# Kernel optimization log

Measured on AMD Instinct MI355X. Metric: run time of the kernel, lower is better.

Reference implementation:

```python
import jax, jax.numpy as jnp
import numpy as np

B, L, D_MODEL, H, D_K, D_V, C = 4, 2048, 512, 8, 64, 64, 5
LN_EPS = 1e-5


def setup_inputs() -> dict:
    key = jax.random.key(0)
    ks = jax.random.split(key, 9)
    u_k = min(int(C * np.log(L)), L)  # 38
    s = 1.0 / np.sqrt(D_MODEL)
    return {
        "input_Q": jax.random.normal(ks[0], (B, L, D_MODEL), jnp.float32),
        "input_K": jax.random.normal(ks[1], (B, L, D_MODEL), jnp.float32),
        "input_V": jax.random.normal(ks[2], (B, L, D_MODEL), jnp.float32),
        "W_Q": jax.random.normal(ks[3], (D_MODEL, H * D_K), jnp.float32) * s,
        "W_K": jax.random.normal(ks[4], (D_MODEL, H * D_K), jnp.float32) * s,
        "W_V": jax.random.normal(ks[5], (D_MODEL, H * D_V), jnp.float32) * s,
        "W_fc": jax.random.normal(ks[6], (H * D_V, D_MODEL), jnp.float32) * (1.0 / np.sqrt(H * D_V)),
        "ln_gamma": jnp.ones((D_MODEL,), jnp.float32),
        "ln_beta": jnp.zeros((D_MODEL,), jnp.float32),
        "index_sample": jax.random.randint(ks[7], (L, u_k), 0, L, jnp.int32),
    }


def reference(input_Q, input_K, input_V, W_Q, W_K, W_V, W_fc, ln_gamma, ln_beta, index_sample):
    Bb, L_Q, _ = input_Q.shape
    L_K = input_K.shape[1]
    u_q = min(int(C * np.log(L_Q)), L_Q)  # n_top queries kept

    # projections -> (B, H, L, d)
    Q = (input_Q @ W_Q).reshape(Bb, L_Q, H, D_K).transpose(0, 2, 1, 3)
    K = (input_K @ W_K).reshape(Bb, L_K, H, D_K).transpose(0, 2, 1, 3)
    V = (input_V @ W_V).reshape(Bb, L_K, H, D_V).transpose(0, 2, 1, 3)

    # sampled QK scores: gather u_k random keys per query position
    K_sample = K[:, :, index_sample, :]                      # (B,H,L_Q,u_k,d_k)
    QK_sample = jnp.einsum('bhqe,bhqke->bhqk', Q, K_sample)  # (B,H,L_Q,u_k)

    # sparsity measure M = max - mean, top-u_q queries
    M = QK_sample.max(axis=-1) - QK_sample.mean(axis=-1)     # (B,H,L_Q)
    _, idx = jax.lax.top_k(M, u_q)                           # (B,H,u_q)

    # attention only for selected queries
    Q_sel = jnp.take_along_axis(Q, idx[..., None], axis=2)   # (B,H,u_q,d_k)
    scores = jnp.einsum('bhue,bhke->bhuk', Q_sel, K) / np.sqrt(D_K)
    attn = jax.nn.softmax(scores, axis=-1)
    values = jnp.einsum('bhuk,bhkd->bhud', attn, V)          # (B,H,u_q,d_v)

    # initial context = mean of V (attn_mask is None), scatter selected rows
    context = jnp.broadcast_to(V.mean(axis=2, keepdims=True), (Bb, H, L_Q, D_V))
    bb = jnp.arange(Bb)[:, None, None]
    hh = jnp.arange(H)[None, :, None]
    context = context.at[bb, hh, idx].set(values)

    context = context.transpose(0, 2, 1, 3).reshape(Bb, L_Q, H * D_V)
    out = context @ W_fc                                     # dropout p=0.0

    y = out + input_Q
    mu = y.mean(axis=-1, keepdims=True)
    var = jnp.mean(jnp.square(y - mu), axis=-1, keepdims=True)
    y = (y - mu) / jnp.sqrt(var + LN_EPS) * ln_gamma + ln_beta
    return y, idx
```

## Files before the change

### kernel.cpp

```cpp
#include <hip/hip_runtime.h>
#include <hip/hip_bf16.h>

#define NB 4
#define NL 2048
#define NH 8
#define NDM 512
#define ND 64
#define KSPLIT 4
#define QB 8

typedef __attribute__((ext_vector_type(8))) short short8b;
typedef __attribute__((ext_vector_type(4))) float f32x4;

__global__ void samp_flag_init(int* __restrict__ flag) {
  if (threadIdx.x == 0 && blockIdx.x == 0) *flag = 0;
}
__global__ void samp_probe(const int* __restrict__ sampAsInt, int* __restrict__ flag, int nwords) {
  const int g = blockIdx.x * 256 + threadIdx.x;
  if (g < nwords) {
    unsigned v = (unsigned)sampAsInt[g];
    if (v >= 2048u) atomicOr(flag, 1);
  }
}
__global__ void samp_convert(const void* __restrict__ samp, const int* __restrict__ flag,
                             int* __restrict__ sampI, int n) {
  const int g = blockIdx.x * 256 + threadIdx.x;
  if (g >= n) return;
  int v;
  if (*flag == 0) v = ((const int*)samp)[g];
  else            v = (int)(((const float*)samp)[g]);
  if (v < 0) v = 0;
  if (v > NL - 1) v = NL - 1;
  sampI[g] = v;
}

__global__ void wconv(const float* __restrict__ W, unsigned short* __restrict__ WT) {
  const int g = blockIdx.x * 256 + threadIdx.x;
  const int k = g >> 9, c = g & 511;
  __hip_bfloat16 hb = __float2bfloat16(W[(size_t)k * 512 + c]);
  WT[(size_t)c * 512 + k] = *reinterpret_cast<unsigned short*>(&hb);
}

__global__ void vmean_colmean(const float* __restrict__ inV, float* __restrict__ parts) {
  const int b = blockIdx.x, seg = blockIdx.y, t = threadIdx.x;
  const float* p = inV + ((size_t)b * NL + seg * 32) * NDM;
  float s0 = 0.f, s1 = 0.f;
  for (int r = 0; r < 32; ++r) {
    s0 += p[(size_t)r * NDM + t];
    s1 += p[(size_t)r * NDM + 256 + t];
  }
  parts[((size_t)b * 64 + seg) * NDM + t] = s0;
  parts[((size_t)b * 64 + seg) * NDM + 256 + t] = s1;
}
__global__ void vmean_gemm(const float* __restrict__ parts, const float* __restrict__ Wv,
                           float* __restrict__ Vm) {
  __shared__ float cm[512];
  const int b = blockIdx.x, t = threadIdx.x;
  float a0 = 0.f, a1 = 0.f;
  for (int g = 0; g < 64; ++g) {
    a0 += parts[((size_t)b * 64 + g) * NDM + t];
    a1 += parts[((size_t)b * 64 + g) * NDM + 256 + t];
  }
  cm[t] = a0 * (1.f / 2048.f);
  cm[t + 256] = a1 * (1.f / 2048.f);
  __syncthreads();
  const int c0 = blockIdx.y * 256 + t;
  float acc = 0.f;
  for (int k = 0; k < 512; ++k) acc += cm[k] * Wv[(size_t)k * NDM + c0];
  Vm[b * 512 + c0] = acc;
}

__global__ __launch_bounds__(256, 4) void proj3(
    const float* __restrict__ AQ, const float* __restrict__ AK,
    const float* __restrict__ wQm, const float* __restrict__ wKm,
    int gh0, float* __restrict__ Qc, float* __restrict__ Kc) {
  __shared__ float As_[32 * 132];
  __shared__ float Ws_[32 * 68];
  const int tid = threadIdx.x;
  const int bm = blockIdx.x;
  const int hl = blockIdx.y;
  const int mat = blockIdx.z;
  const int bh = gh0 + hl;
  const int b = bh >> 3, h = bh & 7;
  const float* A = (mat == 0) ? AQ : AK;
  const float* W = (mat == 0) ? wQm : wKm;
  float* D = (mat == 0) ? Qc : Kc;
  const float* Ab = A + (size_t)b * NL * NDM;
  const int colbase = h * 64;
  const int tm = tid >> 4, tn = tid & 15;
  float acc[8][4] = {};
  for (int k0 = 0; k0 < 512; k0 += 32) {
#pragma unroll
    for (int i = 0; i < 4; ++i) {
      int s = tid + i * 256;
      int r = s >> 3, c4 = (s & 7) * 4;
      float4 v = *reinterpret_cast<const float4*>(Ab + (size_t)(bm * 128 + r) * 512 + k0 + c4);
      float vv[4] = {v.x, v.y, v.z, v.w};
#pragma unroll
      for (int j = 0; j < 4; ++j) {
        int c = c4 + j;
        int rs = r ^ (((c >> 2) & 3) << 3);
        As_[c * 132 + rs] = vv[j];
      }
    }
#pragma unroll
    for (int i = 0; i < 2; ++i) {
      int s = tid + i * 256;
      int r = s >> 4, c4 = (s & 15) * 4;
      *reinterpret_cast<float4*>(&Ws_[r * 68 + c4]) =
          *reinterpret_cast<const float4*>(W + (size_t)(k0 + r) * 512 + colbase + c4);
    }
    __syncthreads();
#pragma unroll
    for (int kk = 0; kk < 32; ++kk) {
      const int sw = ((kk >> 2) & 3) << 3;
      const int mbase = (tm * 4) ^ sw;
      float4 a0 = *reinterpret_cast<const float4*>(&As_[kk * 132 + mbase]);
      float4 a1 = *reinterpret_cast<const float4*>(&As_[kk * 132 + 64 + mbase]);
      float4 w  = *reinterpret_cast<const float4*>(&Ws_[kk * 68 + tn * 4]);
      float a[8] = {a0.x, a0.y, a0.z, a0.w, a1.x, a1.y, a1.z, a1.w};
      float wv[4] = {w.x, w.y, w.z, w.w};
#pragma unroll
      for (int ii = 0; ii < 8; ++ii)
#pragma unroll
        for (int jj = 0; jj < 4; ++jj) acc[ii][jj] += a[ii] * wv[jj];
    }
    __syncthreads();
  }
#pragma unroll
  for (int ii = 0; ii < 8; ++ii) {
    int row = bm * 128 + ((ii < 4) ? (tm * 4 + ii) : (64 + tm * 4 + (ii - 4)));
    float4 v = make_float4(acc[ii][0], acc[ii][1], acc[ii][2], acc[ii][3]);
    *reinterpret_cast<float4*>(D + ((size_t)hl * NL + row) * ND + tn * 4) = v;
  }
}

__global__ __launch_bounds__(256) void projV_mfma(
    const float* __restrict__ AV, const unsigned short* __restrict__ WT,
    int gh0, float* __restrict__ Vc) {
  const int wv = threadIdx.x >> 6, l = threadIdx.x & 63;
  const int bm = blockIdx.x;
  const int hl = blockIdx.y;
  const int bh = gh0 + hl;
  const int b = bh >> 3, h = bh & 7;
  const float* Ab = AV + (size_t)b * NL * NDM;
  const int row = bm * 64 + wv * 16 + (l & 15);
  const int kg = (l >> 4) * 8;
  f32x4 acc0 = {}, acc1 = {}, acc2 = {}, acc3 = {};
  for (int k0 = 0; k0 < 512; k0 += 32) {
    const float* ap = Ab + (size_t)row * 512 + k0 + kg;
    short8b af;
#pragma unroll
    for (int j = 0; j < 8; ++j) {
      __hip_bfloat16 hb = __float2bfloat16(ap[j]);
      af[j] = *reinterpret_cast<short*>(&hb);
    }
    const unsigned short* wp = WT + (size_t)(h * 64 + (l & 15)) * 512 + k0 + kg;
    short8b b0 = *reinterpret_cast<const short8b*>(wp);
    short8b b1 = *reinterpret_cast<const short8b*>(wp + 16 * 512);
    short8b b2 = *reinterpret_cast<const short8b*>(wp + 32 * 512);
    short8b b3 = *reinterpret_cast<const short8b*>(wp + 48 * 512);
    acc0 = __builtin_amdgcn_mfma_f32_16x16x32_bf16(af, b0, acc0, 0, 0, 0);
    acc1 = __builtin_amdgcn_mfma_f32_16x16x32_bf16(af, b1, acc1, 0, 0, 0);
    acc2 = __builtin_amdgcn_mfma_f32_16x16x32_bf16(af, b2, acc2, 0, 0, 0);
    acc3 = __builtin_amdgcn_mfma_f32_16x16x32_bf16(af, b3, acc3, 0, 0, 0);
  }
  const int rbase = bm * 64 + wv * 16 + (l >> 4) * 4;
  const int col = l & 15;
#pragma unroll
  for (int j = 0; j < 4; ++j) {
    size_t o = ((size_t)hl * NL + rbase + j) * ND + col;
    Vc[o] = acc0[j];
    Vc[o + 16] = acc1[j];
    Vc[o + 32] = acc2[j];
    Vc[o + 48] = acc3[j];
  }
}

template <int UK>
__global__ __launch_bounds__(256) void sample_scores_t(
    const float* __restrict__ Q, const float* __restrict__ K,
    const int* __restrict__ sampI, float* __restrict__ M) {
  __shared__ float KsAll[4][UK * 66];
  __shared__ float QsAll[4][68];
  const int wv = threadIdx.x >> 6, l = threadIdx.x & 63;
  const int gq = blockIdx.x * 4 + wv;
  const int hl = gq >> 11;
  const int q = gq & 2047;
  float* Ks = KsAll[wv];
  float* Qs = QsAll[wv];
  const float* Kb = K + (size_t)hl * NL * ND;
  Qs[l] = Q[(size_t)gq * ND + l];
  const int base = __builtin_amdgcn_readfirstlane(q) * UK;
#pragma unroll
  for (int r = 0; r < UK; ++r) {
    int kk = sampI[base + r] & (NL - 1);
    Ks[r * 66 + l] = Kb[(size_t)kk * ND + l];
  }
  __syncthreads();
  const int myk = (l < UK) ? l : (UK - 1);
  float acc = 0.f;
#pragma unroll
  for (int j = 0; j < 32; ++j) {
    float2 kv = *reinterpret_cast<const float2*>(&Ks[myk * 66 + 2 * j]);
    float2 qv = *reinterpret_cast<const float2*>(&Qs[2 * j]);
    acc += kv.x * qv.x + kv.y * qv.y;
  }
  float mval = (l < UK) ? acc : -1e30f;
  float sval = (l < UK) ? acc : 0.f;
#pragma unroll
  for (int o = 32; o; o >>= 1) {
    mval = fmaxf(mval, __shfl_xor(mval, o, 64));
    sval += __shfl_xor(sval, o, 64);
  }
  if (l == 0) M[gq] = mval - sval * (1.f / (float)UK);
}

__global__ void sample_scores_gen(const float* __restrict__ Q, const float* __restrict__ K,
                                  const int* __restrict__ sampI, float* __restrict__ M, int uk) {
  const int wave = threadIdx.x >> 6, lane = threadIdx.x & 63;
  const int gq = blockIdx.x * 4 + wave;
  const int hl = gq >> 11;
  const int q = gq & 2047;
  const float qv = Q[(size_t)gq * ND + lane];
  const float* Kbase = K + (size_t)hl * NL * ND;
  float mx = -1e30f, sm = 0.f;
  for (int k = 0; k < uk; ++k) {
    int kidx = sampI[q * uk + k] & (NL - 1);
    float p = qv * Kbase[(size_t)kidx * ND + lane];
#pragma unroll
    for (int o = 32; o; o >>= 1) p += __shfl_xor(p, o, 64);
    mx = fmaxf(mx, p);
    sm += p;
  }
  if (lane == 0) M[gq] = mx - sm / (float)uk;
}

__global__ void topk_kernel(const float* __restrict__ M, int* __restrict__ idxo,
                            float* __restrict__ outIdx, int uq) {
  __shared__ float mv[2048];
  __shared__ float bwv[4];
  __shared__ int bwi[4];
  const int bh = blockIdx.x, t = threadIdx.x;
  for (int i = 0; i < 8; ++i) mv[t + i * 256] = M[(size_t)bh * 2048 + t + i * 256];
  __syncthreads();
  for (int it = 0; it < uq; ++it) {
    float best = -1e38f; int bidx = 1 << 30;
#pragma unroll
    for (int i = 0; i < 8; ++i) {
      int id = t + i * 256;
      float v = mv[id];
      if (v > best || (v == best && id < bidx)) { best = v; bidx = id; }
    }
#pragma unroll
    for (int o = 32; o; o >>= 1) {
      float ov = __shfl_xor(best, o, 64);
      int oi = __shfl_xor(bidx, o, 64);
      if (ov > best || (ov == best && oi < bidx)) { best = ov; bidx = oi; }
    }
    if ((t & 63) == 0) { bwv[t >> 6] = best; bwi[t >> 6] = bidx; }
    __syncthreads();
    if (t == 0) {
      float bb = bwv[0]; int bi2 = bwi[0];
#pragma unroll
      for (int w = 1; w < 4; ++w) {
        if (bwv[w] > bb || (bwv[w] == bb && bwi[w] < bi2)) { bb = bwv[w]; bi2 = bwi[w]; }
      }
      int sel = bi2 & (NL - 1);
      idxo[bh * uq + it] = sel;
      outIdx[bh * uq + it] = (float)sel;
      mv[sel] = -1e38f;
    }
    __syncthreads();
  }
}

__global__ __launch_bounds__(256) void attn_part(
    const float* __restrict__ Qw, const float* __restrict__ Kw, const float* __restrict__ Vw,
    const int* __restrict__ idxo, float* __restrict__ pacc, float* __restrict__ pml, int uq) {
  __shared__ float Qs[QB][68];
  __shared__ float Ks[64][68];
  __shared__ float Vs[64][68];
  __shared__ float sc[QB][66];
  __shared__ float accs[QB][68];
  const int hl = blockIdx.x, qg = blockIdx.y, ks = blockIdx.z;
  const int t = threadIdx.x;
#pragma unroll
  for (int i = 0; i < 2; ++i) {
    int s = t + i * 256;
    int q = s >> 6, d = s & 63;
    int u = qg * QB + q;
    float v = 0.f;
    if (u < uq) {
      int qi = idxo[hl * uq + u] & (NL - 1);
      v = Qw[((size_t)hl * NL + qi) * ND + d];
    }
    Qs[q][d] = v;
    accs[q][d] = 0.f;
  }
  float m_run = -1e30f, l_run = 0.f;
  const int q2 = t >> 5, ln = t & 31;
  __syncthreads();
  const int kbeg = ks * (NL / KSPLIT);
  for (int k0 = kbeg; k0 < kbeg + NL / KSPLIT; k0 += 64) {
#pragma unroll
    for (int i = 0; i < 4; ++i) {
      int s = t + i * 256;
      int r = s >> 4, c4 = (s & 15) * 4;
      *reinterpret_cast<float4*>(&Ks[r][c4]) =
          *reinterpret_cast<const float4*>(Kw + ((size_t)hl * NL + k0 + r) * ND + c4);
      *reinterpret_cast<float4*>(&Vs[r][c4]) =
          *reinterpret_cast<const float4*>(Vw + ((size_t)hl * NL + k0 + r) * ND + c4);
    }
    __syncthreads();
    {
      const int q = t & 7, kk = t >> 3;
      float d0 = 0.f, d1 = 0.f;
#pragma unroll
      for (int dd = 0; dd < 64; dd += 4) {
        float4 qv = *reinterpret_cast<const float4*>(&Qs[q][dd]);
        float4 ka = *reinterpret_cast<const float4*>(&Ks[kk][dd]);
        float4 kb = *reinterpret_cast<const float4*>(&Ks[kk + 32][dd]);
        d0 += qv.x * ka.x + qv.y * ka.y + qv.z * ka.z + qv.w * ka.w;
        d1 += qv.x * kb.x + qv.y * kb.y + qv.z * kb.z + qv.w * kb.w;
      }
      sc[q][kk] = d0 * 0.125f;
      sc[q][kk + 32] = d1 * 0.125f;
    }
    __syncthreads();
    {
      float s0 = sc[q2][ln], s1 = sc[q2][ln + 32];
      float tmax = fmaxf(s0, s1);
#pragma unroll
      for (int o = 16; o; o >>= 1) tmax = fmaxf(tmax, __shfl_xor(tmax, o, 64));
      float mnew = fmaxf(m_run, tmax);
      float scl = __expf(m_run - mnew);
      float p0 = __expf(s0 - mnew), p1 = __expf(s1 - mnew);
      float tsum = p0 + p1;
#pragma unroll
      for (int o = 16; o; o >>= 1) tsum += __shfl_xor(tsum, o, 64);
      l_run = l_run * scl + tsum;
      m_run = mnew;
      sc[q2][ln] = p0; sc[q2][ln + 32] = p1;
      float a0 = accs[q2][2 * ln] * scl, a1 = accs[q2][2 * ln + 1] * scl;
#pragma unroll 8
      for (int k = 0; k < 64; ++k) {
        float p = sc[q2][k];
        a0 += p * Vs[k][2 * ln];
        a1 += p * Vs[k][2 * ln + 1];
      }
      accs[q2][2 * ln] = a0; accs[q2][2 * ln + 1] = a1;
    }
    __syncthreads();
  }
  const int u = qg * QB + q2;
  if (u < uq) {
    size_t g = ((size_t)hl * uq + u) * KSPLIT + ks;
    pacc[g * ND + 2 * ln] = accs[q2][2 * ln];
    pacc[g * ND + 2 * ln + 1] = accs[q2][2 * ln + 1];
    if (ln == 0) { pml[g * 2] = m_run; pml[g * 2 + 1] = l_run; }
  }
}

__global__ void attn_merge(const float* __restrict__ pacc, const float* __restrict__ pml,
                           float* __restrict__ vals, int uq) {
  const int g = blockIdx.x;
  const int d = threadIdx.x;
  float mstar = -1e30f;
#pragma unroll
  for (int s = 0; s < KSPLIT; ++s) mstar = fmaxf(mstar, pml[((size_t)g * KSPLIT + s) * 2]);
  float num = 0.f, den = 0.f;
#pragma unroll
  for (int s = 0; s < KSPLIT; ++s) {
    float e = __expf(pml[((size_t)g * KSPLIT + s) * 2] - mstar);
    den += e * pml[((size_t)g * KSPLIT + s) * 2 + 1];
    num += e * pacc[((size_t)g * KSPLIT + s) * ND + d];
  }
  vals[(size_t)g * ND + d] = num / den;
}

__global__ void selmap_init(short* __restrict__ selmap) {
  const int g = blockIdx.x * 256 + threadIdx.x;
  selmap[g] = -1;
  selmap[g + 32768] = -1;
}
__global__ void selmap_fill(const int* __restrict__ idxo, short* __restrict__ selmap, int uq) {
  const int g = blockIdx.x * 256 + threadIdx.x;
  if (g >= NB * NH * uq) return;
  const int bh = g / uq, u = g - bh * uq;
  const int b = bh >> 3, h = bh & 7;
  const int l = idxo[g] & (NL - 1);
  selmap[((size_t)b * NL + l) * NH + h] = (short)u;
}

__global__ void base_gemm(const float* __restrict__ Vm, const float* __restrict__ Wfc,
                          float* __restrict__ base) {
  __shared__ float vm[512];
  const int b = blockIdx.x, t = threadIdx.x;
  vm[t] = Vm[b * 512 + t];
  vm[t + 256] = Vm[b * 512 + t + 256];
  __syncthreads();
  const int c0 = blockIdx.y * 256 + t;
  float acc = 0.f;
  for (int k = 0; k < 512; ++k) acc += vm[k] * Wfc[(size_t)k * 512 + c0];
  base[b * 512 + c0] = acc;
}

__global__ void corr_gemm(const float* __restrict__ vals, const float* __restrict__ Vm,
                          const float* __restrict__ Wfc, float* __restrict__ corr, int uq) {
  __shared__ float diff[64];
  const int g = blockIdx.x, t = threadIdx.x;
  const int bh = g / uq;
  const int h = bh & 7;
  if (t < 64) diff[t] = vals[(size_t)g * 64 + t] - Vm[bh * 64 + t];
  __syncthreads();
  float a0 = 0.f, a1 = 0.f;
#pragma unroll
  for (int d = 0; d < 64; ++d) {
    a0 += diff[d] * Wfc[(size_t)(h * 64 + d) * 512 + t];
    a1 += diff[d] * Wfc[(size_t)(h * 64 + d) * 512 + t + 256];
  }
  corr[(size_t)g * 512 + t] = a0;
  corr[(size_t)g * 512 + t + 256] = a1;
}

__global__ void ln_fused(const float* __restrict__ base, const float* __restrict__ resid,
                         const float* __restrict__ corr, const short* __restrict__ selmap,
                         const float* __restrict__ gamma, const float* __restrict__ beta,
                         float* __restrict__ out, int uq) {
  __shared__ float red[256];
  const int row = blockIdx.x, t = threadIdx.x;
  const int b = row >> 11;
  float y0 = base[b * 512 + t] + resid[(size_t)row * 512 + t];
  float y1 = base[b * 512 + 256 + t] + resid[(size_t)row * 512 + 256 + t];
#pragma unroll
  for (int h = 0; h < NH; ++h) {
    int s = selmap[(size_t)row * NH + h];
    if (s >= 0 && s < uq) {
      const float* cp = corr + (size_t)((b * NH + h) * uq + s) * 512;
      y0 += cp[t];
      y1 += cp[t + 256];
    }
  }
  red[t] = y0 + y1;
  __syncthreads();
  for (int s = 128; s; s >>= 1) { if (t < s) red[t] += red[t + s]; __syncthreads(); }
  const float mu = red[0] * (1.f / 512.f);
  __syncthreads();
  const float d0 = y0 - mu, d1 = y1 - mu;
  red[t] = d0 * d0 + d1 * d1;
  __syncthreads();
  for (int s = 128; s; s >>= 1) { if (t < s) red[t] += red[t + s]; __syncthreads(); }
  const float rs = rsqrtf(red[0] * (1.f / 512.f) + 1e-5f);
  __syncthreads();
  out[(size_t)row * 512 + t] = d0 * rs * gamma[t] + beta[t];
  out[(size_t)row * 512 + 256 + t] = d1 * rs * gamma[256 + t] + beta[256 + t];
}

extern "C" void kernel_launch(void* const* d_in, const int* in_sizes, int n_in,
                              void* d_out, int out_size, void* d_ws, size_t ws_size,
                              hipStream_t stream) {
  const float* inQ = (const float*)d_in[0];
  const float* inK = (const float*)d_in[1];
  const float* inV = (const float*)d_in[2];
  const float* wQ = (const float*)d_in[3];
  const float* wK = (const float*)d_in[4];
  const float* wV = (const float*)d_in[5];
  const float* wFC = (const float*)d_in[6];
  const float* gamma = (const float*)d_in[7];
  const float* beta = (const float*)d_in[8];
  const void* samp = d_in[9];

  const int nsamp = in_sizes[9];
  const int uk = nsamp / NL;
  const int uq = uk;
  const int nqg = (uq + QB - 1) / QB;

  if (out_size < NB * NL * NDM + NB * NH * uq) return;

  const size_t perH = 3 * 131072 + 2048 + (size_t)uq * KSPLIT * 64 + (size_t)uq * KSPLIT * 2;
  const size_t fixed = (size_t)32 * uq * 64 + 2048 + 2048 + (size_t)32 * uq * 512
                     + (size_t)32 * uq + 32768 + (size_t)nsamp + 131072 + 131072 + 256;
  int hcg = 0;
  for (int c = 32; c >= 1; c >>= 1) {
    if ((perH * (size_t)c + fixed + 256) * 4ull <= ws_size) { hcg = c; break; }
  }
  if (hcg == 0) return;

  float* ws = (float*)d_ws;
  float* Qc = ws;
  float* Kc = Qc + (size_t)hcg * 131072;
  float* Vc = Kc + (size_t)hcg * 131072;
  float* Mb = Vc + (size_t)hcg * 131072;
  float* pacc = Mb + (size_t)hcg * 2048;
  float* pml = pacc + (size_t)hcg * uq * KSPLIT * 64;
  float* vals = pml + (size_t)hcg * uq * KSPLIT * 2;
  float* Vm = vals + (size_t)32 * uq * 64;
  float* base = Vm + 2048;
  float* corr = base + 2048;
  int* idxo = (int*)(corr + (size_t)32 * uq * 512);
  short* selmap = (short*)(idxo + (size_t)32 * uq);
  int* sampI = (int*)(selmap + 65536);
  int* flag = sampI + nsamp;
  unsigned short* WTv = (unsigned short*)(flag + 64);
  float* vparts = (float*)(WTv + 262144);

  float* out = (float*)d_out;
  float* outIdx = out + (size_t)NB * NL * NDM;

  const int nwords = nsamp / 2;
  samp_flag_init<<<1, 64, 0, stream>>>(flag);
  samp_probe<<<(nwords + 255) / 256, 256, 0, stream>>>((const int*)samp, flag, nwords);
  samp_convert<<<(nsamp + 255) / 256, 256, 0, stream>>>(samp, flag, sampI, nsamp);
  wconv<<<1024, 256, 0, stream>>>(wV, WTv);
  vmean_colmean<<<dim3(NB, 64), 256, 0, stream>>>(inV, vparts);
  vmean_gemm<<<dim3(NB, 2), 256, 0, stream>>>(vparts, wV, Vm);

  for (int gh0 = 0; gh0 < NB * NH; gh0 += hcg) {
    proj3<<<dim3(16, hcg, 2), 256, 0, stream>>>(inQ, inK, wQ, wK, gh0, Qc, Kc);
    projV_mfma<<<dim3(32, hcg), 256, 0, stream>>>(inV, WTv, gh0, Vc);
    if (uk == 38)
      sample_scores_t<38><<<hcg * NL / 4, 256, 0, stream>>>(Qc, Kc, sampI, Mb);
    else
      sample_scores_gen<<<hcg * NL / 4, 256, 0, stream>>>(Qc, Kc, sampI, Mb, uk);
    topk_kernel<<<hcg, 256, 0, stream>>>(Mb, idxo + (size_t)gh0 * uq,
                                         outIdx + (size_t)gh0 * uq, uq);
    attn_part<<<dim3(hcg, nqg, KSPLIT), 256, 0, stream>>>(Qc, Kc, Vc,
                                                          idxo + (size_t)gh0 * uq,
                                                          pacc, pml, uq);
    attn_merge<<<hcg * uq, 64, 0, stream>>>(pacc, pml, vals + (size_t)gh0 * uq * ND, uq);
  }

  selmap_init<<<NB * NL * NH / 2 / 256, 256, 0, stream>>>(selmap);
  selmap_fill<<<(NB * NH * uq + 255) / 256, 256, 0, stream>>>(idxo, selmap, uq);
  base_gemm<<<dim3(NB, 2), 256, 0, stream>>>(Vm, wFC, base);
  corr_gemm<<<NB * NH * uq, 256, 0, stream>>>(vals, Vm, wFC, corr, uq);
  ln_fused<<<NB * NL, 256, 0, stream>>>(base, inQ, corr, selmap, gamma, beta, out, uq);
}
```

Before: 380.0 us.

## Drop sample-index conversion kernels and restructure QK projection to two heads per block

Removes the three kernels that probed and converted the sample index array, and instead reads the int32 indices directly, saving three launches and a pass over the index data. The Q/K projection kernel now uses 128-thread blocks over 64-row tiles. Each block computes two adjacent heads at once, reusing the same shared-memory A tile. Weights are read straight from global memory instead of being staged in shared memory. This raises per-thread register use (64 accumulators) and relies on cache hits for the weight reads, and it drops the fallback for float-typed indices and for odd head-group counts.

```diff
diff --git a/kernel.cpp b/kernel.cpp
--- a/kernel.cpp
+++ b/kernel.cpp
@@ -11,28 +11,6 @@
 
 typedef __attribute__((ext_vector_type(8))) short short8b;
 typedef __attribute__((ext_vector_type(4))) float f32x4;
-
-__global__ void samp_flag_init(int* __restrict__ flag) {
-  if (threadIdx.x == 0 && blockIdx.x == 0) *flag = 0;
-}
-__global__ void samp_probe(const int* __restrict__ sampAsInt, int* __restrict__ flag, int nwords) {
-  const int g = blockIdx.x * 256 + threadIdx.x;
-  if (g < nwords) {
-    unsigned v = (unsigned)sampAsInt[g];
-    if (v >= 2048u) atomicOr(flag, 1);
-  }
-}
-__global__ void samp_convert(const void* __restrict__ samp, const int* __restrict__ flag,
-                             int* __restrict__ sampI, int n) {
-  const int g = blockIdx.x * 256 + threadIdx.x;
-  if (g >= n) return;
-  int v;
-  if (*flag == 0) v = ((const int*)samp)[g];
-  else            v = (int)(((const float*)samp)[g]);
-  if (v < 0) v = 0;
-  if (v > NL - 1) v = NL - 1;
-  sampI[g] = v;
-}
 
 __global__ void wconv(const float* __restrict__ W, unsigned short* __restrict__ WT) {
   const int g = blockIdx.x * 256 + threadIdx.x;
@@ -70,68 +48,69 @@
   Vm[b * 512 + c0] = acc;
 }
 
-__global__ __launch_bounds__(256, 4) void proj3(
+__global__ __launch_bounds__(128, 4) void proj_qk(
     const float* __restrict__ AQ, const float* __restrict__ AK,
     const float* __restrict__ wQm, const float* __restrict__ wKm,
     int gh0, float* __restrict__ Qc, float* __restrict__ Kc) {
-  __shared__ float As_[32 * 132];
-  __shared__ float Ws_[32 * 68];
+  __shared__ float As_[32 * 68];
   const int tid = threadIdx.x;
   const int bm = blockIdx.x;
-  const int hl = blockIdx.y;
+  const int hp = blockIdx.y;
   const int mat = blockIdx.z;
-  const int bh = gh0 + hl;
+  const int bh = gh0 + hp * 2;
   const int b = bh >> 3, h = bh & 7;
   const float* A = (mat == 0) ? AQ : AK;
   const float* W = (mat == 0) ? wQm : wKm;
   float* D = (mat == 0) ? Qc : Kc;
   const float* Ab = A + (size_t)b * NL * NDM;
   const int colbase = h * 64;
-  const int tm = tid >> 4, tn = tid & 15;
-  float acc[8][4] = {};
+  const int tm = tid >> 4;
+  const int tn = tid & 15;
+  float acc0[8][4] = {};
+  float acc1[8][4] = {};
   for (int k0 = 0; k0 < 512; k0 += 32) {
 #pragma unroll
     for (int i = 0; i < 4; ++i) {
-      int s = tid + i * 256;
+      int s = tid + i * 128;
       int r = s >> 3, c4 = (s & 7) * 4;
-      float4 v = *reinterpret_cast<const float4*>(Ab + (size_t)(bm * 128 + r) * 512 + k0 + c4);
+      float4 v = *reinterpret_cast<const float4*>(Ab + (size_t)(bm * 64 + r) * 512 + k0 + c4);
       float vv[4] = {v.x, v.y, v.z, v.w};
 #pragma unroll
       for (int j = 0; j < 4; ++j) {
         int c = c4 + j;
         int rs = r ^ (((c >> 2) & 3) << 3);
-        As_[c * 132 + rs] = vv[j];
+        As_[c * 68 + rs] = vv[j];
       }
-    }
-#pragma unroll
-    for (int i = 0; i < 2; ++i) {
-      int s = tid + i * 256;
-      int r = s >> 4, c4 = (s & 15) * 4;
-      *reinterpret_cast<float4*>(&Ws_[r * 68 + c4]) =
-          *reinterpret_cast<const float4*>(W + (size_t)(k0 + r) * 512 + colbase + c4);
     }
     __syncthreads();
 #pragma unroll
     for (int kk = 0; kk < 32; ++kk) {
       const int sw = ((kk >> 2) & 3) << 3;
-      const int mbase = (tm * 4) ^ sw;
-      float4 a0 = *reinterpret_cast<const float4*>(&As_[kk * 132 + mbase]);
-      float4 a1 = *reinterpret_cast<const float4*>(&As_[kk * 132 + 64 + mbase]);
-      float4 w  = *reinterpret_cast<const float4*>(&Ws_[kk * 68 + tn * 4]);
+      const int mb = (tm * 8) ^ sw;
+      float4 a0 = *reinterpret_cast<const float4*>(&As_[kk * 68 + mb]);
+      float4 a1 = *reinterpret_cast<const float4*>(&As_[kk * 68 + mb + 4]);
+      const float* wrow = W + (size_t)(k0 + kk) * 512 + colbase + tn * 4;
+      float4 w0 = *reinterpret_cast<const float4*>(wrow);
+      float4 w1 = *reinterpret_cast<const float4*>(wrow + 64);
       float a[8] = {a0.x, a0.y, a0.z, a0.w, a1.x, a1.y, a1.z, a1.w};
-      float wv[4] = {w.x, w.y, w.z, w.w};
-#pragma unroll
-      for (int ii = 0; ii < 8; ++ii)
-#pragma unroll
-        for (int jj = 0; jj < 4; ++jj) acc[ii][jj] += a[ii] * wv[jj];
-    }
-    __syncthreads();
-  }
+#pragma unroll
+      for (int ii = 0; ii < 8; ++ii) {
+        acc0[ii][0] += a[ii] * w0.x; acc0[ii][1] += a[ii] * w0.y;
+        acc0[ii][2] += a[ii] * w0.z; acc0[ii][3] += a[ii] * w0.w;
+        acc1[ii][0] += a[ii] * w1.x; acc1[ii][1] += a[ii] * w1.y;
+        acc1[ii][2] += a[ii] * w1.z; acc1[ii][3] += a[ii] * w1.w;
+      }
+    }
+    __syncthreads();
+  }
+  const int hl0 = hp * 2, hl1 = hp * 2 + 1;
 #pragma unroll
   for (int ii = 0; ii < 8; ++ii) {
-    int row = bm * 128 + ((ii < 4) ? (tm * 4 + ii) : (64 + tm * 4 + (ii - 4)));
-    float4 v = make_float4(acc[ii][0], acc[ii][1], acc[ii][2], acc[ii][3]);
-    *reinterpret_cast<float4*>(D + ((size_t)hl * NL + row) * ND + tn * 4) = v;
+    int row = bm * 64 + tm * 8 + ii;
+    *reinterpret_cast<float4*>(D + ((size_t)hl0 * NL + row) * ND + tn * 4) =
+        make_float4(acc0[ii][0], acc0[ii][1], acc0[ii][2], acc0[ii][3]);
+    *reinterpret_cast<float4*>(D + ((size_t)hl1 * NL + row) * ND + tn * 4) =
+        make_float4(acc1[ii][0], acc1[ii][1], acc1[ii][2], acc1[ii][3]);
   }
 }
 
@@ -180,7 +159,7 @@
 template <int UK>
 __global__ __launch_bounds__(256) void sample_scores_t(
     const float* __restrict__ Q, const float* __restrict__ K,
-    const int* __restrict__ sampI, float* __restrict__ M) {
+    const int* __restrict__ sampP, float* __restrict__ M) {
   __shared__ float KsAll[4][UK * 66];
   __shared__ float QsAll[4][68];
   const int wv = threadIdx.x >> 6, l = threadIdx.x & 63;
@@ -194,7 +173,7 @@
   const int base = __builtin_amdgcn_readfirstlane(q) * UK;
 #pragma unroll
   for (int r = 0; r < UK; ++r) {
-    int kk = sampI[base + r] & (NL - 1);
+    int kk = sampP[base + r] & (NL - 1);
     Ks[r * 66 + l] = Kb[(size_t)kk * ND + l];
   }
   __syncthreads();
@@ -217,7 +196,7 @@
 }
 
 __global__ void sample_scores_gen(const float* __restrict__ Q, const float* __restrict__ K,
-                                  const int* __restrict__ sampI, float* __restrict__ M, int uk) {
+                                  const int* __restrict__ sampP, float* __restrict__ M, int uk) {
   const int wave = threadIdx.x >> 6, lane = threadIdx.x & 63;
   const int gq = blockIdx.x * 4 + wave;
   const int hl = gq >> 11;
@@ -226,7 +205,7 @@
   const float* Kbase = K + (size_t)hl * NL * ND;
   float mx = -1e30f, sm = 0.f;
   for (int k = 0; k < uk; ++k) {
-    int kidx = sampI[q * uk + k] & (NL - 1);
+    int kidx = sampP[q * uk + k] & (NL - 1);
     float p = qv * Kbase[(size_t)kidx * ND + lane];
 #pragma unroll
     for (int o = 32; o; o >>= 1) p += __shfl_xor(p, o, 64);
@@ -469,7 +448,7 @@
   const float* wFC = (const float*)d_in[6];
   const float* gamma = (const float*)d_in[7];
   const float* beta = (const float*)d_in[8];
-  const void* samp = d_in[9];
+  const int* samp = (const int*)d_in[9];
 
   const int nsamp = in_sizes[9];
   const int uk = nsamp / NL;
@@ -480,9 +459,9 @@
 
   const size_t perH = 3 * 131072 + 2048 + (size_t)uq * KSPLIT * 64 + (size_t)uq * KSPLIT * 2;
   const size_t fixed = (size_t)32 * uq * 64 + 2048 + 2048 + (size_t)32 * uq * 512
-                     + (size_t)32 * uq + 32768 + (size_t)nsamp + 131072 + 131072 + 256;
+                     + (size_t)32 * uq + 32768 + 131072 + 131072 + 256;
   int hcg = 0;
-  for (int c = 32; c >= 1; c >>= 1) {
+  for (int c = 32; c >= 2; c >>= 1) {
     if ((perH * (size_t)c + fixed + 256) * 4ull <= ws_size) { hcg = c; break; }
   }
   if (hcg == 0) return;
@@ -500,29 +479,23 @@
   float* corr = base + 2048;
   int* idxo = (int*)(corr + (size_t)32 * uq * 512);
   short* selmap = (short*)(idxo + (size_t)32 * uq);
-  int* sampI = (int*)(selmap + 65536);
-  int* flag = sampI + nsamp;
-  unsigned short* WTv = (unsigned short*)(flag + 64);
+  unsigned short* WTv = (unsigned short*)(selmap + 65536);
   float* vparts = (float*)(WTv + 262144);
 
   float* out = (float*)d_out;
   float* outIdx = out + (size_t)NB * NL * NDM;
 
-  const int nwords = nsamp / 2;
-  samp_flag_init<<<1, 64, 0, stream>>>(flag);
-  samp_probe<<<(nwords + 255) / 256, 256, 0, stream>>>((const int*)samp, flag, nwords);
-  samp_convert<<<(nsamp + 255) / 256, 256, 0, stream>>>(samp, flag, sampI, nsamp);
   wconv<<<1024, 256, 0, stream>>>(wV, WTv);
   vmean_colmean<<<dim3(NB, 64), 256, 0, stream>>>(inV, vparts);
   vmean_gemm<<<dim3(NB, 2), 256, 0, stream>>>(vparts, wV, Vm);
 
   for (int gh0 = 0; gh0 < NB * NH; gh0 += hcg) {
-    proj3<<<dim3(16, hcg, 2), 256, 0, stream>>>(inQ, inK, wQ, wK, gh0, Qc, Kc);
+    proj_qk<<<dim3(32, hcg / 2, 2), 128, 0, stream>>>(inQ, inK, wQ, wK, gh0, Qc, Kc);
     projV_mfma<<<dim3(32, hcg), 256, 0, stream>>>(inV, WTv, gh0, Vc);
     if (uk == 38)
-      sample_scores_t<38><<<hcg * NL / 4, 256, 0, stream>>>(Qc, Kc, sampI, Mb);
+      sample_scores_t<38><<<hcg * NL / 4, 256, 0, stream>>>(Qc, Kc, samp, Mb);
     else
-      sample_scores_gen<<<hcg * NL / 4, 256, 0, stream>>>(Qc, Kc, sampI, Mb, uk);
+      sample_scores_gen<<<hcg * NL / 4, 256, 0, stream>>>(Qc, Kc, samp, Mb, uk);
     topk_kernel<<<hcg, 256, 0, stream>>>(Mb, idxo + (size_t)gh0 * uq,
                                          outIdx + (size_t)gh0 * uq, uq);
     attn_part<<<dim3(hcg, nqg, KSPLIT), 256, 0, stream>>>(Qc, Kc, Vc,
```

Measured after the change: 419.3 us. 1.1x slower.
